# Optimization experiments

Measured on AMD Instinct MI355X. Metric: run time of the kernel, lower is better.

Reference implementation:

```python
import jax, jax.numpy as jnp
import numpy as np

N_EMBED = 768
NUM_EXPERTS = 8
TOP_K = 2
B, S = 2, 2048
THRESH = 1e-09


def setup_inputs() -> dict:
    key = jax.random.key(0)
    ks = jax.random.split(key, 12)
    d, e, f = N_EMBED, NUM_EXPERTS, 4 * N_EMBED
    s_in = 1.0 / np.sqrt(d)
    s_hid = 1.0 / np.sqrt(f)
    return {
        'x': jax.random.normal(ks[0], (B, S, d), jnp.float32),
        'noise': jax.random.normal(ks[1], (B * S, e), jnp.float32),
        'Wg': jax.random.normal(ks[2], (d, e), jnp.float32) * s_in,
        'bg': jnp.zeros((e,), jnp.float32),
        'Wn': jax.random.normal(ks[3], (d, e), jnp.float32) * s_in,
        'bn': jnp.zeros((e,), jnp.float32),
        'W1': jax.random.normal(ks[4], (e, d, f), jnp.float32) * s_in,
        'b1': jnp.zeros((e, f), jnp.float32),
        'W2': jax.random.normal(ks[5], (e, f, d), jnp.float32) * s_hid,
        'b2': jnp.zeros((e, d), jnp.float32),
    }


def reference(x, noise, Wg, bg, Wn, bn, W1, b1, W2, b2):
    Bsz, Ssz, d = x.shape
    T = Bsz * Ssz
    xr = x.reshape(T, d)  # [T, d]

    # Noisy top-k router
    logits = xr @ Wg + bg                     # [T, E]
    noise_logits = xr @ Wn + bn               # [T, E]
    noisy = logits + noise * jax.nn.softplus(noise_logits)
    vals, idx = jax.lax.top_k(noisy, TOP_K)   # [T, K]
    rows = jnp.arange(T)[:, None]
    sparse = jnp.full_like(noisy, -jnp.inf).at[rows, idx].set(vals)
    probs = jax.nn.softmax(sparse, axis=-1)   # [T, E]; zeros off top-k

    # Gate = prob masked by activation threshold (matches torch dispatch)
    gate = jnp.where(probs > THRESH, probs, 0.0)  # [T, E]

    # Dense per-expert MLP (dropout=0 -> identity), combined by gate
    h = jax.nn.relu(jnp.einsum('td,edf->etf', xr, W1) + b1[:, None, :])  # [E, T, 4d]
    y = jnp.einsum('etf,efd->etd', h, W2) + b2[:, None, :]               # [E, T, d]
    out = jnp.einsum('te,etd->td', gate, y)                              # [T, d]
    return out.reshape(Bsz, Ssz, d)
```

## Files before the change

### kernel.cpp

```cpp
#include <hip/hip_runtime.h>
#include <math.h>

typedef unsigned short u16;
typedef unsigned int u32;

#define D_EMB 768
#define F_HID 3072
#define N_TOK 4096
#define N_PAIR 8192
#define GATE_TH 1e-9f

typedef float f32x4 __attribute__((ext_vector_type(4)));
typedef __bf16 bfrag __attribute__((ext_vector_type(8)));
typedef u16 u16x8 __attribute__((ext_vector_type(8)));

__device__ inline float b2f(u16 u) {
    union { float f; u32 i; } c; c.i = ((u32)u) << 16; return c.f;
}
__device__ inline u16 f2b(float f) {
    union { float f; u32 i; } c; c.f = f;
    u32 r = c.i + 0x7FFFu + ((c.i >> 16) & 1u);
    return (u16)(r >> 16);
}
__device__ inline f32x4 mfma16(bfrag a, bfrag b, f32x4 c) {
    return __builtin_amdgcn_mfma_f32_16x16x32_bf16(a, b, c, 0, 0, 0);
}
__device__ inline void gll16(const u16* g, u16* l) {
    __builtin_amdgcn_global_load_lds(
        (const __attribute__((address_space(1))) u32*)g,
        (__attribute__((address_space(3))) u32*)l, 16, 0, 0);
}
__device__ inline void sbar() {
    asm volatile("" ::: "memory");
    __builtin_amdgcn_s_barrier();
    asm volatile("" ::: "memory");
}
__device__ inline void waitv0() { asm volatile("s_waitcnt vmcnt(0)" ::: "memory"); }
__device__ inline void waitv6() { asm volatile("s_waitcnt vmcnt(6)" ::: "memory"); }
__device__ inline void waitv8() { asm volatile("s_waitcnt vmcnt(8)" ::: "memory"); }

__global__ __launch_bounds__(256) void moe_zero_kernel(uint4* __restrict__ out) {
    int i = blockIdx.x * 256 + threadIdx.x;
    out[i] = make_uint4(0, 0, 0, 0);
}

__global__ __launch_bounds__(64) void moe_router_v4(
    const float* __restrict__ x, const float* __restrict__ noise,
    const float* __restrict__ Wg, const float* __restrict__ bg,
    const float* __restrict__ Wn, const float* __restrict__ bn,
    int* __restrict__ tk_e, float* __restrict__ tk_g,
    ushort4* __restrict__ xb4)
{
    const int lane = threadIdx.x;
    const int tl = lane & 7, q = lane >> 3;
    const int t = blockIdx.x * 8 + tl;
    float ag[8] = {}, an[8] = {};
    const float4* xp = (const float4*)(x + (size_t)t * D_EMB + q * 96);
#pragma unroll 4
    for (int k4 = 0; k4 < 24; k4++) {
        float4 xv = xp[k4];
        const int kb = q * 96 + k4 * 4;
#pragma unroll
        for (int c = 0; c < 4; c++) {
            float xc = (&xv.x)[c];
            const float4* wg = (const float4*)(Wg + (size_t)(kb + c) * 8);
            const float4* wn = (const float4*)(Wn + (size_t)(kb + c) * 8);
            float4 g0 = wg[0], g1 = wg[1], n0 = wn[0], n1 = wn[1];
            ag[0] += xc * g0.x; ag[1] += xc * g0.y; ag[2] += xc * g0.z; ag[3] += xc * g0.w;
            ag[4] += xc * g1.x; ag[5] += xc * g1.y; ag[6] += xc * g1.z; ag[7] += xc * g1.w;
            an[0] += xc * n0.x; an[1] += xc * n0.y; an[2] += xc * n0.z; an[3] += xc * n0.w;
            an[4] += xc * n1.x; an[5] += xc * n1.y; an[6] += xc * n1.z; an[7] += xc * n1.w;
        }
    }
#pragma unroll
    for (int e = 0; e < 8; e++) {
        ag[e] += __shfl_xor(ag[e], 8);  an[e] += __shfl_xor(an[e], 8);
        ag[e] += __shfl_xor(ag[e], 16); an[e] += __shfl_xor(an[e], 16);
        ag[e] += __shfl_xor(ag[e], 32); an[e] += __shfl_xor(an[e], 32);
    }
    if (q == 0) {
        float best = -INFINITY, sec = -INFINITY; int be = 0, se = 0;
#pragma unroll
        for (int e = 0; e < 8; e++) {
            float nl = an[e] + bn[e];
            float sp = nl > 0.f ? nl + log1pf(expf(-nl)) : log1pf(expf(nl));
            float v = ag[e] + bg[e] + noise[(size_t)t * 8 + e] * sp;
            if (v > best) { sec = best; se = be; best = v; be = e; }
            else if (v > sec) { sec = v; se = e; }
        }
        float ex = expf(sec - best);
        float g1 = 1.f / (1.f + ex), g2 = ex / (1.f + ex);
        tk_e[t * 2 + 0] = (g1 > GATE_TH) ? be : -1; tk_g[t * 2 + 0] = g1;
        tk_e[t * 2 + 1] = (g2 > GATE_TH) ? se : -1; tk_g[t * 2 + 1] = g2;
    }
    if (xb4) {
        const int t0 = blockIdx.x * 8;
        for (int i = lane; i < 8 * 192; i += 64) {
            int ti = i / 192, c = i - ti * 192;
            float4 v = *(const float4*)(x + (size_t)(t0 + ti) * D_EMB + c * 4);
            ushort4 o;
            o.x = f2b(v.x); o.y = f2b(v.y); o.z = f2b(v.z); o.w = f2b(v.w);
            xb4[(size_t)(t0 + ti) * 192 + c] = o;
        }
    }
}

__global__ __launch_bounds__(256) void moe_plan_kernel(
    const int* __restrict__ tk_e, const float* __restrict__ tk_g,
    int* __restrict__ cnt, int* __restrict__ off,
    int* __restrict__ plist, float* __restrict__ pg, int* __restrict__ pos)
{
    __shared__ int lc[8 * 256];
    __shared__ int ob[8];
    const int t = threadIdx.x;
#pragma unroll
    for (int e = 0; e < 8; e++) lc[e * 256 + t] = 0;
    __syncthreads();
    const int i0 = t * 32;
    for (int j = 0; j < 32; j++) {
        int e = tk_e[i0 + j];
        if (e >= 0) lc[e * 256 + t]++;
    }
    __syncthreads();
    if (t < 8) {
        int s = 0;
        for (int u = 0; u < 256; u++) {
            int v = lc[t * 256 + u]; lc[t * 256 + u] = s; s += v;
        }
        ob[t] = s;
    }
    __syncthreads();
    if (t == 0) {
        int s = 0;
        for (int e = 0; e < 8; e++) {
            int v = ob[e]; cnt[e] = v; off[e] = s; ob[e] = s; s += v;
        }
    }
    __syncthreads();
    for (int j = 0; j < 32; j++) {
        int e = tk_e[i0 + j];
        if (e >= 0) {
            int p = ob[e] + lc[e * 256 + t]++;
            plist[p] = (i0 + j) >> 1;
            pg[p] = tk_g[i0 + j];
            pos[i0 + j] = p;
        }
    }
}

__global__ __launch_bounds__(256) void moe_transcvt_kernel(
    const float* __restrict__ in, u16* __restrict__ out, int R, int C) {
    __shared__ float tile[64][65];
    const int z = blockIdx.z;
    const int c0 = blockIdx.x * 64, r0 = blockIdx.y * 64;
    const size_t base = (size_t)z * R * C;
    const int t = threadIdx.x;
    {
        const int row = t >> 2, cb = (t & 3) * 16;
        const float* src = in + base + (size_t)(r0 + row) * C + c0 + cb;
        float4 v0 = ((const float4*)src)[0];
        float4 v1 = ((const float4*)src)[1];
        float4 v2 = ((const float4*)src)[2];
        float4 v3 = ((const float4*)src)[3];
        float* d = &tile[row][cb];
        d[0]  = v0.x; d[1]  = v0.y; d[2]  = v0.z; d[3]  = v0.w;
        d[4]  = v1.x; d[5]  = v1.y; d[6]  = v1.z; d[7]  = v1.w;
        d[8]  = v2.x; d[9]  = v2.y; d[10] = v2.z; d[11] = v2.w;
        d[12] = v3.x; d[13] = v3.y; d[14] = v3.z; d[15] = v3.w;
    }
    __syncthreads();
    const int c = t >> 2, rb = (t & 3) * 16;
    u16x8 o0, o1;
#pragma unroll
    for (int i = 0; i < 8; i++) o0[i] = f2b(tile[rb + i][c]);
#pragma unroll
    for (int i = 0; i < 8; i++) o1[i] = f2b(tile[rb + 8 + i][c]);
    u16* dst = out + base + (size_t)(c0 + c) * R + r0 + rb;
    *(u16x8*)dst = o0;
    *(u16x8*)(dst + 8) = o1;
}

__global__ __launch_bounds__(256) void moe_ffn1_kernel(
    const u16* __restrict__ xb, const u16* __restrict__ wt, const float* __restrict__ b1,
    const int* __restrict__ plist, const int* __restrict__ cnt, const int* __restrict__ off,
    u16* __restrict__ h, int P0, int P1)
{
    __shared__ __align__(16) u16 As[2][128 * 64];
    __shared__ __align__(16) u16 Bs[2][128 * 64];
    const int GX = 24, GY = 16;
    int f = blockIdx.x + GX * (blockIdx.y + GY * blockIdx.z);
    int swz = (f & 7) * 384 + (f >> 3);
    int nb = swz % GX;
    int t2 = swz / GX;
    int mb = t2 % GY;
    int e  = t2 / GY;

    int lo = off[e], hi = lo + cnt[e];
    if (lo < P0) lo = P0;
    if (hi > P1) hi = P1;
    const int Cl = hi - lo;
    if (Cl <= 0) return;
    const int n0 = nb * 128;
    const int tid = threadIdx.x;
    const int lane = tid & 63, wave = tid >> 6;
    const int wr = wave >> 1, wc = wave & 1;
    const int qq = lane >> 4, r = lane & 15;
    const int srow = tid >> 3;
    const int gq = (tid & 7) ^ (srow & 7);

    const u16* bsrc[4];
#pragma unroll
    for (int j = 0; j < 4; j++)
        bsrc[j] = wt + ((size_t)e * F_HID + n0 + j * 32 + srow) * D_EMB + gq * 8;

    for (int m0 = mb * 128; m0 < Cl; m0 += GY * 128) {
        const u16* asrc[4];
#pragma unroll
        for (int j = 0; j < 4; j++) {
            int mr = m0 + j * 32 + srow;
            if (mr > Cl - 1) mr = Cl - 1;
            asrc[j] = xb + (size_t)plist[lo + mr] * D_EMB + gq * 8;
        }
        f32x4 acc[4][4] = {};

        auto stage = [&](int kt, int buf) {
            const int k0 = kt * 64;
#pragma unroll
            for (int j = 0; j < 4; j++)
                gll16(asrc[j] + k0, &As[buf][j * 2048 + wave * 512]);
#pragma unroll
            for (int j = 0; j < 4; j++)
                gll16(bsrc[j] + k0, &Bs[buf][j * 2048 + wave * 512]);
        };
        auto compute = [&](int buf) {
#pragma unroll
            for (int kk = 0; kk < 2; kk++) {
                bfrag af[4], bf[4];
#pragma unroll
                for (int i = 0; i < 4; i++) {
                    int rowa = wr * 64 + i * 16 + r;
                    int rowb = wc * 64 + i * 16 + r;
                    int slot = ((qq + 4 * kk) ^ (r & 7)) * 8;
                    af[i] = *(const bfrag*)(&As[buf][rowa * 64 + slot]);
                    bf[i] = *(const bfrag*)(&Bs[buf][rowb * 64 + slot]);
                }
#pragma unroll
                for (int mi = 0; mi < 4; mi++)
#pragma unroll
                    for (int ni = 0; ni < 4; ni++)
                        acc[mi][ni] = mfma16(af[mi], bf[ni], acc[mi][ni]);
            }
        };

        waitv0();
        stage(0, 0);
        for (int kt = 0; kt < 11; kt++) {
            stage(kt + 1, (kt + 1) & 1);
            waitv8(); sbar();
            compute(kt & 1);
            sbar();
        }
        waitv0(); sbar();
        compute(1);

#pragma unroll
        for (int mi = 0; mi < 4; mi++)
#pragma unroll
            for (int ni = 0; ni < 4; ni++) {
                int col = n0 + wc * 64 + ni * 16 + r;
                float bias = b1[(size_t)e * F_HID + col];
#pragma unroll
                for (int i = 0; i < 4; i++) {
                    int m = m0 + wr * 64 + mi * 16 + qq * 4 + i;
                    if (m < Cl) {
                        float v = acc[mi][ni][i] + bias;
                        h[(size_t)(lo - P0 + m) * F_HID + col] = f2b(v > 0.f ? v : 0.f);
                    }
                }
            }
    }
}

__global__ __launch_bounds__(256) void moe_ffn2_kernel(
    const u16* __restrict__ h, const u16* __restrict__ wt, const float* __restrict__ b2,
    const int* __restrict__ cnt, const int* __restrict__ off,
    float* __restrict__ y, int P0, int P1)
{
    __shared__ __align__(16) u16 As[2][64 * 64];
    __shared__ __align__(16) u16 Bs[2][128 * 64];
    const int GX = 6, GY = 32;
    int f = blockIdx.x + GX * (blockIdx.y + GY * blockIdx.z);
    int swz = (f & 7) * 192 + (f >> 3);
    int nb = swz % GX;
    int t2 = swz / GX;
    int mb = t2 % GY;
    int e  = t2 / GY;

    int lo = off[e], hi = lo + cnt[e];
    if (lo < P0) lo = P0;
    if (hi > P1) hi = P1;
    const int Cl = hi - lo;
    if (Cl <= 0) return;
    const int n0 = nb * 128;
    const int tid = threadIdx.x;
    const int lane = tid & 63, wave = tid >> 6;
    const int wr = wave >> 1, wc = wave & 1;
    const int qq = lane >> 4, r = lane & 15;
    const int srow = tid >> 3;
    const int gq = (tid & 7) ^ (srow & 7);
    const int hcap = P1 - P0;

    const u16* bsrc[4];
#pragma unroll
    for (int j = 0; j < 4; j++)
        bsrc[j] = wt + ((size_t)e * D_EMB + n0 + j * 32 + srow) * F_HID + gq * 8;

    for (int m0 = mb * 64; m0 < Cl; m0 += GY * 64) {
        const u16* asrc[2];
#pragma unroll
        for (int j = 0; j < 2; j++) {
            int mr = m0 + j * 32 + srow;
            if (mr > Cl - 1) mr = Cl - 1;
            asrc[j] = h + (size_t)(lo - P0 + ((mr < hcap) ? mr : hcap - 1)) * F_HID + gq * 8;
        }
        f32x4 acc[2][4] = {};

        auto stage = [&](int kt, int buf) {
            const int k0 = kt * 64;
#pragma unroll
            for (int j = 0; j < 2; j++)
                gll16(asrc[j] + k0, &As[buf][j * 2048 + wave * 512]);
#pragma unroll
            for (int j = 0; j < 4; j++)
                gll16(bsrc[j] + k0, &Bs[buf][j * 2048 + wave * 512]);
        };
        auto compute = [&](int buf) {
#pragma unroll
            for (int kk = 0; kk < 2; kk++) {
                bfrag af[2], bf[4];
#pragma unroll
                for (int i = 0; i < 2; i++) {
                    int rowa = wr * 32 + i * 16 + r;
                    int slot = ((qq + 4 * kk) ^ (r & 7)) * 8;
                    af[i] = *(const bfrag*)(&As[buf][rowa * 64 + slot]);
                }
#pragma unroll
                for (int i = 0; i < 4; i++) {
                    int rowb = wc * 64 + i * 16 + r;
                    int slot = ((qq + 4 * kk) ^ (r & 7)) * 8;
                    bf[i] = *(const bfrag*)(&Bs[buf][rowb * 64 + slot]);
                }
#pragma unroll
                for (int mi = 0; mi < 2; mi++)
#pragma unroll
                    for (int ni = 0; ni < 4; ni++)
                        acc[mi][ni] = mfma16(af[mi], bf[ni], acc[mi][ni]);
            }
        };

        waitv0();
        stage(0, 0);
        for (int kt = 0; kt < 47; kt++) {
            stage(kt + 1, (kt + 1) & 1);
            waitv6(); sbar();
            compute(kt & 1);
            sbar();
        }
        waitv0(); sbar();
        compute(1);

#pragma unroll
        for (int mi = 0; mi < 2; mi++)
#pragma unroll
            for (int ni = 0; ni < 4; ni++) {
                int col = n0 + wc * 64 + ni * 16 + r;
                float bias = b2[(size_t)e * D_EMB + col];
#pragma unroll
                for (int i = 0; i < 4; i++) {
                    int m = m0 + wr * 32 + mi * 16 + qq * 4 + i;
                    if (m < Cl)
                        y[(size_t)(lo + m) * D_EMB + col] = acc[mi][ni][i] + bias;
                }
            }
    }
}

__global__ __launch_bounds__(256) void moe_combine_kernel(
    const float* __restrict__ y, const int* __restrict__ tk_e,
    const float* __restrict__ tk_g, const int* __restrict__ pos,
    float4* __restrict__ out)
{
    int i = blockIdx.x * 256 + threadIdx.x;
    int t = i / 192;
    int c = i - t * 192;
    float4 a = make_float4(0.f, 0.f, 0.f, 0.f);
#pragma unroll
    for (int k = 0; k < 2; k++) {
        int e = tk_e[t * 2 + k];
        if (e >= 0) {
            float g = tk_g[t * 2 + k];
            float4 v = ((const float4*)(y + (size_t)pos[t * 2 + k] * D_EMB))[c];
            a.x += g * v.x; a.y += g * v.y; a.z += g * v.z; a.w += g * v.w;
        }
    }
    out[i] = a;
}

#define XSTR 776
#define HSTR 3080
#define BMF 8
__global__ __launch_bounds__(256) void moe_ffn_fused_f32(
    const float* __restrict__ x,
    const float* __restrict__ w1, const float* __restrict__ b1,
    const float* __restrict__ w2, const float* __restrict__ b2,
    const int* __restrict__ plist, const float* __restrict__ pg,
    const int* __restrict__ cnt, const int* __restrict__ off,
    float* __restrict__ out)
{
    __shared__ __align__(16) u16 xs[BMF * XSTR];
    __shared__ __align__(16) u16 hs[BMF * HSTR];
    const int e = blockIdx.x;
    const int Cl = cnt[e];
    if (Cl <= 0) return;
    const int O = off[e];
    const int tid = threadIdx.x;
    for (int t0 = blockIdx.y * BMF; t0 < Cl; t0 += gridDim.y * BMF) {
        for (int ci = tid; ci < BMF * 192; ci += 256) {
            int row = ci / 192, c = ci - row * 192;
            float4 v = make_float4(0.f, 0.f, 0.f, 0.f);
            if (t0 + row < Cl) {
                int tok = plist[O + t0 + row];
                v = *(const float4*)(x + (size_t)tok * D_EMB + c * 4);
            }
            u16* d = &xs[row * XSTR + c * 4];
            d[0] = f2b(v.x); d[1] = f2b(v.y); d[2] = f2b(v.z); d[3] = f2b(v.w);
        }
        __syncthreads();
        for (int wi = tid; wi < BMF * 768; wi += 256) {
            int row = wi / 768, nc = wi - row * 768;
            int n0 = nc * 4;
            float a0 = 0, a1 = 0, a2 = 0, a3 = 0;
            const float* wp = w1 + (size_t)e * D_EMB * F_HID + n0;
            const u16* xr = &xs[row * XSTR];
            for (int k = 0; k < D_EMB; k++) {
                float4 wv = *(const float4*)(wp + (size_t)k * F_HID);
                float xv = b2f(xr[k]);
                a0 += xv * wv.x; a1 += xv * wv.y; a2 += xv * wv.z; a3 += xv * wv.w;
            }
            const float* bp = b1 + (size_t)e * F_HID + n0;
            u16* hp = &hs[row * HSTR + n0];
            float v;
            v = a0 + bp[0]; hp[0] = f2b(v > 0.f ? v : 0.f);
            v = a1 + bp[1]; hp[1] = f2b(v > 0.f ? v : 0.f);
            v = a2 + bp[2]; hp[2] = f2b(v > 0.f ? v : 0.f);
            v = a3 + bp[3]; hp[3] = f2b(v > 0.f ? v : 0.f);
        }
        __syncthreads();
        for (int wi = tid; wi < BMF * 192; wi += 256) {
            int row = wi / 192, nc = wi - row * 192;
            int n0 = nc * 4;
            float a0 = 0, a1 = 0, a2 = 0, a3 = 0;
            const float* wp = w2 + (size_t)e * F_HID * D_EMB + n0;
            const u16* hr = &hs[row * HSTR];
            for (int k = 0; k < F_HID; k++) {
                float4 wv = *(const float4*)(wp + (size_t)k * D_EMB);
                float hv = b2f(hr[k]);
                a0 += hv * wv.x; a1 += hv * wv.y; a2 += hv * wv.z; a3 += hv * wv.w;
            }
            if (t0 + row < Cl) {
                int p = O + t0 + row;
                int tok = plist[p];
                float g = pg[p];
                const float* bp = b2 + (size_t)e * D_EMB + n0;
                float* op = out + (size_t)tok * D_EMB + n0;
                atomicAdd(&op[0], g * (a0 + bp[0]));
                atomicAdd(&op[1], g * (a1 + bp[1]));
                atomicAdd(&op[2], g * (a2 + bp[2]));
                atomicAdd(&op[3], g * (a3 + bp[3]));
            }
        }
        __syncthreads();
    }
}

extern "C" void kernel_launch(void* const* d_in, const int* in_sizes, int n_in,
                              void* d_out, int out_size, void* d_ws, size_t ws_size,
                              hipStream_t stream) {
    const float* x     = (const float*)d_in[0];
    const float* noise = (const float*)d_in[1];
    const float* Wg    = (const float*)d_in[2];
    const float* bg    = (const float*)d_in[3];
    const float* Wn    = (const float*)d_in[4];
    const float* bn    = (const float*)d_in[5];
    const float* W1    = (const float*)d_in[6];
    const float* b1    = (const float*)d_in[7];
    const float* W2    = (const float*)d_in[8];
    const float* b2    = (const float*)d_in[9];
    float* out = (float*)d_out;

    char* ws = (char*)d_ws;
    int*   cnt    = (int*)(ws + 0);
    int*   off    = (int*)(ws + 256);
    int*   tk_e   = (int*)(ws + 1024);
    float* tk_g   = (float*)(ws + 33792);
    int*   plist  = (int*)(ws + 66560);
    float* pg     = (float*)(ws + 99328);
    int*   pos    = (int*)(ws + 132096);
    const size_t SMALL  = 164864;
    const size_t WSZ    = 37748736ull;
    const size_t XB_SZ  = 6291456ull;
    const size_t Y_SZ   = 25165824ull;
    const size_t H_FULL = 50331648ull;

    const size_t NEED_A = SMALL + WSZ + XB_SZ + Y_SZ + H_FULL;

    if (ws_size >= NEED_A) {
        u16*   wt = (u16*)(ws + SMALL);
        u16*   xb = (u16*)(ws + SMALL + WSZ);
        float* y  = (float*)(ws + SMALL + WSZ + XB_SZ);
        u16*   h  = (u16*)(ws + SMALL + WSZ + XB_SZ + Y_SZ);

        moe_router_v4<<<dim3(512), dim3(64), 0, stream>>>(
            x, noise, Wg, bg, Wn, bn, tk_e, tk_g, (ushort4*)xb);
        moe_plan_kernel<<<dim3(1), dim3(256), 0, stream>>>(
            tk_e, tk_g, cnt, off, plist, pg, pos);
        moe_transcvt_kernel<<<dim3(F_HID / 64, D_EMB / 64, 8), dim3(256), 0, stream>>>(
            W1, wt, D_EMB, F_HID);
        moe_ffn1_kernel<<<dim3(24, 16, 8), dim3(256), 0, stream>>>(
            xb, wt, b1, plist, cnt, off, h, 0, N_PAIR);
        moe_transcvt_kernel<<<dim3(D_EMB / 64, F_HID / 64, 8), dim3(256), 0, stream>>>(
            W2, wt, F_HID, D_EMB);
        moe_ffn2_kernel<<<dim3(6, 32, 8), dim3(256), 0, stream>>>(
            h, wt, b2, cnt, off, y, 0, N_PAIR);
        moe_combine_kernel<<<dim3(3072), dim3(256), 0, stream>>>(
            y, tk_e, tk_g, pos, (float4*)out);
        (void)in_sizes; (void)n_in; (void)out_size;
        return;
    }

    const size_t B_BASE = SMALL + 2 * WSZ + XB_SZ + Y_SZ;
    int pchunk = 0;
    for (int p = N_PAIR; p >= 512; p >>= 1) {
        if (B_BASE + (size_t)p * F_HID * 2 <= ws_size) { pchunk = p; break; }
    }

    moe_router_v4<<<dim3(512), dim3(64), 0, stream>>>(
        x, noise, Wg, bg, Wn, bn, tk_e, tk_g,
        pchunk > 0 ? (ushort4*)(ws + SMALL + 2 * WSZ) : (ushort4*)0);
    moe_plan_kernel<<<dim3(1), dim3(256), 0, stream>>>(
        tk_e, tk_g, cnt, off, plist, pg, pos);

    if (pchunk > 0) {
        u16*   w1t = (u16*)(ws + SMALL);
        u16*   w2t = (u16*)(ws + SMALL + WSZ);
        u16*   xb  = (u16*)(ws + SMALL + 2 * WSZ);
        float* y   = (float*)(ws + SMALL + 2 * WSZ + XB_SZ);
        u16*   h   = (u16*)(ws + B_BASE);
        moe_transcvt_kernel<<<dim3(F_HID / 64, D_EMB / 64, 8), dim3(256), 0, stream>>>(
            W1, w1t, D_EMB, F_HID);
        moe_transcvt_kernel<<<dim3(D_EMB / 64, F_HID / 64, 8), dim3(256), 0, stream>>>(
            W2, w2t, F_HID, D_EMB);
        for (int c = 0; c < N_PAIR / pchunk; c++) {
            int P0 = c * pchunk, P1 = P0 + pchunk;
            moe_ffn1_kernel<<<dim3(24, 16, 8), dim3(256), 0, stream>>>(
                xb, w1t, b1, plist, cnt, off, h, P0, P1);
            moe_ffn2_kernel<<<dim3(6, 32, 8), dim3(256), 0, stream>>>(
                h, w2t, b2, cnt, off, y, P0, P1);
        }
        moe_combine_kernel<<<dim3(3072), dim3(256), 0, stream>>>(
            y, tk_e, tk_g, pos, (float4*)out);
    } else {
        moe_zero_kernel<<<dim3(3072), dim3(256), 0, stream>>>((uint4*)out);
        moe_ffn_fused_f32<<<dim3(8, 192), dim3(256), 0, stream>>>(
            x, W1, b1, W2, b2, plist, pg, cnt, off, out);
    }
    (void)in_sizes; (void)n_in; (void)out_size;
}
```

Measured before the change: 414.0 us.

## Deepen FFN GEMM pipelines to four stages with K-tile of 32

After: 463.9 us. 12.1% more time.

```diff
diff --git a/kernel.cpp b/kernel.cpp
--- a/kernel.cpp
+++ b/kernel.cpp
@@ -35,9 +35,13 @@
     __builtin_amdgcn_s_barrier();
     asm volatile("" ::: "memory");
 }
-__device__ inline void waitv0() { asm volatile("s_waitcnt vmcnt(0)" ::: "memory"); }
-__device__ inline void waitv6() { asm volatile("s_waitcnt vmcnt(6)" ::: "memory"); }
-__device__ inline void waitv8() { asm volatile("s_waitcnt vmcnt(8)" ::: "memory"); }
+__device__ inline void waitv0()  { asm volatile("s_waitcnt vmcnt(0)"  ::: "memory"); }
+__device__ inline void waitv3()  { asm volatile("s_waitcnt vmcnt(3)"  ::: "memory"); }
+__device__ inline void waitv4()  { asm volatile("s_waitcnt vmcnt(4)"  ::: "memory"); }
+__device__ inline void waitv6()  { asm volatile("s_waitcnt vmcnt(6)"  ::: "memory"); }
+__device__ inline void waitv8()  { asm volatile("s_waitcnt vmcnt(8)"  ::: "memory"); }
+__device__ inline void waitv9()  { asm volatile("s_waitcnt vmcnt(9)"  ::: "memory"); }
+__device__ inline void waitv12() { asm volatile("s_waitcnt vmcnt(12)" ::: "memory"); }
 
 __global__ __launch_bounds__(256) void moe_zero_kernel(uint4* __restrict__ out) {
     int i = blockIdx.x * 256 + threadIdx.x;
@@ -185,8 +189,8 @@
     const int* __restrict__ plist, const int* __restrict__ cnt, const int* __restrict__ off,
     u16* __restrict__ h, int P0, int P1)
 {
-    __shared__ __align__(16) u16 As[2][128 * 64];
-    __shared__ __align__(16) u16 Bs[2][128 * 64];
+    __shared__ __align__(16) u16 As[4][128 * 32];
+    __shared__ __align__(16) u16 Bs[4][128 * 32];
     const int GX = 24, GY = 16;
     int f = blockIdx.x + GX * (blockIdx.y + GY * blockIdx.z);
     int swz = (f & 7) * 384 + (f >> 3);
@@ -205,63 +209,52 @@
     const int lane = tid & 63, wave = tid >> 6;
     const int wr = wave >> 1, wc = wave & 1;
     const int qq = lane >> 4, r = lane & 15;
-    const int srow = tid >> 3;
-    const int gq = (tid & 7) ^ (srow & 7);
-
-    const u16* bsrc[4];
-#pragma unroll
-    for (int j = 0; j < 4; j++)
-        bsrc[j] = wt + ((size_t)e * F_HID + n0 + j * 32 + srow) * D_EMB + gq * 8;
+    const int qa = (qq ^ ((r >> 1) & 3)) * 8;
+    const int srow = tid >> 2;
+    const int gq = (tid & 3) ^ ((tid >> 3) & 3);
+
+    const u16* bsrc0 = wt + ((size_t)e * F_HID + n0 + srow) * D_EMB + gq * 8;
+    const u16* bsrc1 = bsrc0 + (size_t)64 * D_EMB;
 
     for (int m0 = mb * 128; m0 < Cl; m0 += GY * 128) {
-        const u16* asrc[4];
-#pragma unroll
-        for (int j = 0; j < 4; j++) {
-            int mr = m0 + j * 32 + srow;
-            if (mr > Cl - 1) mr = Cl - 1;
-            asrc[j] = xb + (size_t)plist[lo + mr] * D_EMB + gq * 8;
-        }
+        int mr0 = m0 + srow;      if (mr0 > Cl - 1) mr0 = Cl - 1;
+        int mr1 = m0 + 64 + srow; if (mr1 > Cl - 1) mr1 = Cl - 1;
+        const u16* asrc0 = xb + (size_t)plist[lo + mr0] * D_EMB + gq * 8;
+        const u16* asrc1 = xb + (size_t)plist[lo + mr1] * D_EMB + gq * 8;
         f32x4 acc[4][4] = {};
 
         auto stage = [&](int kt, int buf) {
-            const int k0 = kt * 64;
-#pragma unroll
-            for (int j = 0; j < 4; j++)
-                gll16(asrc[j] + k0, &As[buf][j * 2048 + wave * 512]);
-#pragma unroll
-            for (int j = 0; j < 4; j++)
-                gll16(bsrc[j] + k0, &Bs[buf][j * 2048 + wave * 512]);
+            const int k0 = kt * 32;
+            gll16(asrc0 + k0, &As[buf][wave * 512]);
+            gll16(asrc1 + k0, &As[buf][2048 + wave * 512]);
+            gll16(bsrc0 + k0, &Bs[buf][wave * 512]);
+            gll16(bsrc1 + k0, &Bs[buf][2048 + wave * 512]);
         };
         auto compute = [&](int buf) {
-#pragma unroll
-            for (int kk = 0; kk < 2; kk++) {
-                bfrag af[4], bf[4];
-#pragma unroll
-                for (int i = 0; i < 4; i++) {
-                    int rowa = wr * 64 + i * 16 + r;
-                    int rowb = wc * 64 + i * 16 + r;
-                    int slot = ((qq + 4 * kk) ^ (r & 7)) * 8;
-                    af[i] = *(const bfrag*)(&As[buf][rowa * 64 + slot]);
-                    bf[i] = *(const bfrag*)(&Bs[buf][rowb * 64 + slot]);
-                }
-#pragma unroll
-                for (int mi = 0; mi < 4; mi++)
-#pragma unroll
-                    for (int ni = 0; ni < 4; ni++)
-                        acc[mi][ni] = mfma16(af[mi], bf[ni], acc[mi][ni]);
-            }
+            bfrag af[4], bf[4];
+#pragma unroll
+            for (int i = 0; i < 4; i++) {
+                af[i] = *(const bfrag*)(&As[buf][(wr * 64 + i * 16 + r) * 32 + qa]);
+                bf[i] = *(const bfrag*)(&Bs[buf][(wc * 64 + i * 16 + r) * 32 + qa]);
+            }
+#pragma unroll
+            for (int mi = 0; mi < 4; mi++)
+#pragma unroll
+                for (int ni = 0; ni < 4; ni++)
+                    acc[mi][ni] = mfma16(af[mi], bf[ni], acc[mi][ni]);
         };
 
         waitv0();
-        stage(0, 0);
-        for (int kt = 0; kt < 11; kt++) {
-            stage(kt + 1, (kt + 1) & 1);
-            waitv8(); sbar();
-            compute(kt & 1);
+        stage(0, 0); stage(1, 1); stage(2, 2);
+        for (int kt = 0; kt < 21; kt++) {
+            stage(kt + 3, (kt + 3) & 3);
+            waitv12(); sbar();
+            compute(kt & 3);
             sbar();
         }
-        waitv0(); sbar();
-        compute(1);
+        waitv8(); sbar(); compute(1); sbar();
+        waitv4(); sbar(); compute(2); sbar();
+        waitv0(); sbar(); compute(3); sbar();
 
 #pragma unroll
         for (int mi = 0; mi < 4; mi++)
@@ -278,6 +271,7 @@
                     }
                 }
             }
+        sbar();
     }
 }
 
@@ -286,8 +280,8 @@
     const int* __restrict__ cnt, const int* __restrict__ off,
     float* __restrict__ y, int P0, int P1)
 {
-    __shared__ __align__(16) u16 As[2][64 * 64];
-    __shared__ __align__(16) u16 Bs[2][128 * 64];
+    __shared__ __align__(16) u16 As[4][64 * 32];
+    __shared__ __align__(16) u16 Bs[4][128 * 32];
     const int GX = 6, GY = 32;
     int f = blockIdx.x + GX * (blockIdx.y + GY * blockIdx.z);
     int swz = (f & 7) * 192 + (f >> 3);
@@ -306,68 +300,53 @@
     const int lane = tid & 63, wave = tid >> 6;
     const int wr = wave >> 1, wc = wave & 1;
     const int qq = lane >> 4, r = lane & 15;
-    const int srow = tid >> 3;
-    const int gq = (tid & 7) ^ (srow & 7);
+    const int qa = (qq ^ ((r >> 1) & 3)) * 8;
+    const int srow = tid >> 2;
+    const int gq = (tid & 3) ^ ((tid >> 3) & 3);
     const int hcap = P1 - P0;
 
-    const u16* bsrc[4];
-#pragma unroll
-    for (int j = 0; j < 4; j++)
-        bsrc[j] = wt + ((size_t)e * D_EMB + n0 + j * 32 + srow) * F_HID + gq * 8;
+    const u16* bsrc0 = wt + ((size_t)e * D_EMB + n0 + srow) * F_HID + gq * 8;
+    const u16* bsrc1 = bsrc0 + (size_t)64 * F_HID;
 
     for (int m0 = mb * 64; m0 < Cl; m0 += GY * 64) {
-        const u16* asrc[2];
-#pragma unroll
-        for (int j = 0; j < 2; j++) {
-            int mr = m0 + j * 32 + srow;
-            if (mr > Cl - 1) mr = Cl - 1;
-            asrc[j] = h + (size_t)(lo - P0 + ((mr < hcap) ? mr : hcap - 1)) * F_HID + gq * 8;
-        }
+        int mr0 = m0 + srow;
+        if (mr0 > Cl - 1) mr0 = Cl - 1;
+        if (mr0 >= hcap) mr0 = hcap - 1;
+        const u16* asrc0 = h + (size_t)(lo - P0 + mr0) * F_HID + gq * 8;
         f32x4 acc[2][4] = {};
 
         auto stage = [&](int kt, int buf) {
-            const int k0 = kt * 64;
-#pragma unroll
-            for (int j = 0; j < 2; j++)
-                gll16(asrc[j] + k0, &As[buf][j * 2048 + wave * 512]);
-#pragma unroll
-            for (int j = 0; j < 4; j++)
-                gll16(bsrc[j] + k0, &Bs[buf][j * 2048 + wave * 512]);
+            const int k0 = kt * 32;
+            gll16(asrc0 + k0, &As[buf][wave * 512]);
+            gll16(bsrc0 + k0, &Bs[buf][wave * 512]);
+            gll16(bsrc1 + k0, &Bs[buf][2048 + wave * 512]);
         };
         auto compute = [&](int buf) {
-#pragma unroll
-            for (int kk = 0; kk < 2; kk++) {
-                bfrag af[2], bf[4];
-#pragma unroll
-                for (int i = 0; i < 2; i++) {
-                    int rowa = wr * 32 + i * 16 + r;
-                    int slot = ((qq + 4 * kk) ^ (r & 7)) * 8;
-                    af[i] = *(const bfrag*)(&As[buf][rowa * 64 + slot]);
-                }
-#pragma unroll
-                for (int i = 0; i < 4; i++) {
-                    int rowb = wc * 64 + i * 16 + r;
-                    int slot = ((qq + 4 * kk) ^ (r & 7)) * 8;
-                    bf[i] = *(const bfrag*)(&Bs[buf][rowb * 64 + slot]);
-                }
-#pragma unroll
-                for (int mi = 0; mi < 2; mi++)
-#pragma unroll
-                    for (int ni = 0; ni < 4; ni++)
-                        acc[mi][ni] = mfma16(af[mi], bf[ni], acc[mi][ni]);
-            }
+            bfrag af[2], bf[4];
+#pragma unroll
+            for (int i = 0; i < 2; i++)
+                af[i] = *(const bfrag*)(&As[buf][(wr * 32 + i * 16 + r) * 32 + qa]);
+#pragma unroll
+            for (int i = 0; i < 4; i++)
+                bf[i] = *(const bfrag*)(&Bs[buf][(wc * 64 + i * 16 + r) * 32 + qa]);
+#pragma unroll
+            for (int mi = 0; mi < 2; mi++)
+#pragma unroll
+                for (int ni = 0; ni < 4; ni++)
+                    acc[mi][ni] = mfma16(af[mi], bf[ni], acc[mi][ni]);
         };
 
         waitv0();
-        stage(0, 0);
-        for (int kt = 0; kt < 47; kt++) {
-            stage(kt + 1, (kt + 1) & 1);
-            waitv6(); sbar();
-            compute(kt & 1);
+        stage(0, 0); stage(1, 1); stage(2, 2);
+        for (int kt = 0; kt < 93; kt++) {
+            stage(kt + 3, (kt + 3) & 3);
+            waitv9(); sbar();
+            compute(kt & 3);
             sbar();
         }
-        waitv0(); sbar();
-        compute(1);
+        waitv6(); sbar(); compute(1); sbar();
+        waitv3(); sbar(); compute(2); sbar();
+        waitv0(); sbar(); compute(3); sbar();
 
 #pragma unroll
         for (int mi = 0; mi < 2; mi++)
@@ -382,6 +361,7 @@
                         y[(size_t)(lo + m) * D_EMB + col] = acc[mi][ni][i] + bias;
                 }
             }
+        sbar();
     }
 }
 
```

## Use triple-buffered K=32 tiles in FFN2 GEMM to drop one barrier per step

Applied to the files above, without the earlier changes.

Measured after the change: 416.0 us. About the same (+0.5%).

```diff
diff --git a/kernel.cpp b/kernel.cpp
--- a/kernel.cpp
+++ b/kernel.cpp
@@ -35,9 +35,9 @@
     __builtin_amdgcn_s_barrier();
     asm volatile("" ::: "memory");
 }
-__device__ inline void waitv0() { asm volatile("s_waitcnt vmcnt(0)" ::: "memory"); }
-__device__ inline void waitv6() { asm volatile("s_waitcnt vmcnt(6)" ::: "memory"); }
-__device__ inline void waitv8() { asm volatile("s_waitcnt vmcnt(8)" ::: "memory"); }
+__device__ inline void waitv0()  { asm volatile("s_waitcnt vmcnt(0)"  ::: "memory"); }
+__device__ inline void waitv3()  { asm volatile("s_waitcnt vmcnt(3)"  ::: "memory"); }
+__device__ inline void waitv8()  { asm volatile("s_waitcnt vmcnt(8)"  ::: "memory"); }
 
 __global__ __launch_bounds__(256) void moe_zero_kernel(uint4* __restrict__ out) {
     int i = blockIdx.x * 256 + threadIdx.x;
@@ -286,8 +286,8 @@
     const int* __restrict__ cnt, const int* __restrict__ off,
     float* __restrict__ y, int P0, int P1)
 {
-    __shared__ __align__(16) u16 As[2][64 * 64];
-    __shared__ __align__(16) u16 Bs[2][128 * 64];
+    __shared__ __align__(16) u16 As[3][64 * 32];
+    __shared__ __align__(16) u16 Bs[3][128 * 32];
     const int GX = 6, GY = 32;
     int f = blockIdx.x + GX * (blockIdx.y + GY * blockIdx.z);
     int swz = (f & 7) * 192 + (f >> 3);
@@ -306,68 +306,54 @@
     const int lane = tid & 63, wave = tid >> 6;
     const int wr = wave >> 1, wc = wave & 1;
     const int qq = lane >> 4, r = lane & 15;
-    const int srow = tid >> 3;
-    const int gq = (tid & 7) ^ (srow & 7);
+    const int qa = (qq ^ ((r >> 1) & 3)) * 8;
+    const int srow = tid >> 2;
+    const int gq = (tid & 3) ^ ((tid >> 3) & 3);
     const int hcap = P1 - P0;
 
-    const u16* bsrc[4];
-#pragma unroll
-    for (int j = 0; j < 4; j++)
-        bsrc[j] = wt + ((size_t)e * D_EMB + n0 + j * 32 + srow) * F_HID + gq * 8;
+    const u16* bsrc0 = wt + ((size_t)e * D_EMB + n0 + srow) * F_HID + gq * 8;
+    const u16* bsrc1 = bsrc0 + (size_t)64 * F_HID;
 
     for (int m0 = mb * 64; m0 < Cl; m0 += GY * 64) {
-        const u16* asrc[2];
-#pragma unroll
-        for (int j = 0; j < 2; j++) {
-            int mr = m0 + j * 32 + srow;
-            if (mr > Cl - 1) mr = Cl - 1;
-            asrc[j] = h + (size_t)(lo - P0 + ((mr < hcap) ? mr : hcap - 1)) * F_HID + gq * 8;
-        }
+        int mr0 = m0 + srow;
+        if (mr0 > Cl - 1) mr0 = Cl - 1;
+        if (mr0 >= hcap) mr0 = hcap - 1;
+        const u16* asrc0 = h + (size_t)(lo - P0 + mr0) * F_HID + gq * 8;
         f32x4 acc[2][4] = {};
 
         auto stage = [&](int kt, int buf) {
-            const int k0 = kt * 64;
-#pragma unroll
-            for (int j = 0; j < 2; j++)
-                gll16(asrc[j] + k0, &As[buf][j * 2048 + wave * 512]);
-#pragma unroll
-            for (int j = 0; j < 4; j++)
-                gll16(bsrc[j] + k0, &Bs[buf][j * 2048 + wave * 512]);
+            const int k0 = kt * 32;
+            gll16(asrc0 + k0, &As[buf][wave * 512]);
+            gll16(bsrc0 + k0, &Bs[buf][wave * 512]);
+            gll16(bsrc1 + k0, &Bs[buf][2048 + wave * 512]);
         };
         auto compute = [&](int buf) {
-#pragma unroll
-            for (int kk = 0; kk < 2; kk++) {
-                bfrag af[2], bf[4];
-#pragma unroll
-                for (int i = 0; i < 2; i++) {
-                    int rowa = wr * 32 + i * 16 + r;
-                    int slot = ((qq + 4 * kk) ^ (r & 7)) * 8;
-                    af[i] = *(const bfrag*)(&As[buf][rowa * 64 + slot]);
-                }
-#pragma unroll
-                for (int i = 0; i < 4; i++) {
-                    int rowb = wc * 64 + i * 16 + r;
-                    int slot = ((qq + 4 * kk) ^ (r & 7)) * 8;
-                    bf[i] = *(const bfrag*)(&Bs[buf][rowb * 64 + slot]);
-                }
-#pragma unroll
-                for (int mi = 0; mi < 2; mi++)
-#pragma unroll
-                    for (int ni = 0; ni < 4; ni++)
-                        acc[mi][ni] = mfma16(af[mi], bf[ni], acc[mi][ni]);
-            }
+            bfrag af[2], bf[4];
+#pragma unroll
+            for (int i = 0; i < 2; i++)
+                af[i] = *(const bfrag*)(&As[buf][(wr * 32 + i * 16 + r) * 32 + qa]);
+#pragma unroll
+            for (int i = 0; i < 4; i++)
+                bf[i] = *(const bfrag*)(&Bs[buf][(wc * 64 + i * 16 + r) * 32 + qa]);
+#pragma unroll
+            for (int mi = 0; mi < 2; mi++)
+#pragma unroll
+                for (int ni = 0; ni < 4; ni++)
+                    acc[mi][ni] = mfma16(af[mi], bf[ni], acc[mi][ni]);
         };
 
         waitv0();
         stage(0, 0);
-        for (int kt = 0; kt < 47; kt++) {
-            stage(kt + 1, (kt + 1) & 1);
-            waitv6(); sbar();
-            compute(kt & 1);
-            sbar();
+        int cb = 0, sb = 1;
+        for (int kt = 0; kt < 95; kt++) {
+            stage(kt + 1, sb);
+            waitv3(); sbar();
+            compute(cb);
+            cb = (cb == 2) ? 0 : cb + 1;
+            sb = (sb == 2) ? 0 : sb + 1;
         }
         waitv0(); sbar();
-        compute(1);
+        compute(cb);
 
 #pragma unroll
         for (int mi = 0; mi < 2; mi++)
@@ -382,6 +368,7 @@
                         y[(size_t)(lo + m) * D_EMB + col] = acc[mi][ni][i] + bias;
                 }
             }
+        sbar();
     }
 }
 
```
